# Kernel tuning notes

Hardware: AMD Instinct MI355X
Metric: run time of the kernel (lower is better)

Reference implementation:

```python
import jax, jax.numpy as jnp
import numpy as np

LMAX = 2
C1 = 64; C2 = 64; COUT = 64
B = 4096
SUM_RDIM = sum(3**L for L in range(LMAX + 1))   # 13
FEAT1 = C1 * SUM_RDIM                            # 832
FEAT2 = C2 * SUM_RDIM


def _enumerate_paths(Lmax):
    paths = []
    for L1 in range(Lmax + 1):
        for L2 in range(Lmax + 1):
            for k in range(min(L1, L2) + 1):
                Lout = L1 + L2 - 2 * k
                if 0 <= Lout <= Lmax:
                    paths.append((L1, L2, Lout, k, False))
            if L1 >= 1 and L2 >= 1:
                for k in range(min(L1 - 1, L2 - 1) + 1):
                    Lout = L1 + L2 - 2 * k - 1
                    if 0 <= Lout <= Lmax:
                        paths.append((L1, L2, Lout, k, True))
    return paths

PATHS = _enumerate_paths(LMAX)   # 15 paths for Lmax=2


def _path_eq(L1, L2, k, use_eps):
    # Fused equation: W[c,a,b] contracted together with the delta/eps path einsum.
    letters = list('defghijklmnopqrstuvwxyz')  # a,b,c reserved for channels
    i_idx = letters[:L1]
    j_idx = letters[L1:L1 + L2]
    for r in range(k):  # delta: contract last k indices of A with last k of B
        j_idx[L2 - k + r] = i_idx[L1 - k + r]
    i_free = i_idx[:L1 - k]
    j_free = j_idx[:L2 - k]
    eps_sub = None
    if use_eps:  # consume last free index of each side via eps_{p i j}
        p = letters[L1 + L2]
        eps_sub = p + i_free[-1] + j_free[-1]
        i_free, j_free = i_free[:-1], j_free[:-1]
        out = i_free + j_free + [p]
    else:
        out = i_free + j_free
    terms = ['cab', '...a' + ''.join(i_idx), '...b' + ''.join(j_idx)]
    if eps_sub is not None:
        terms.append(eps_sub)
    return ','.join(terms) + '->...c' + ''.join(out)


def _epsilon():
    e = np.zeros((3, 3, 3), dtype=np.float32)
    e[0, 1, 2] = e[1, 2, 0] = e[2, 0, 1] = 1.0
    e[2, 1, 0] = e[1, 0, 2] = e[0, 2, 1] = -1.0
    return jnp.asarray(e)


def _split_by_rank(x, C, Lmax):
    batch = x.shape[:-1]
    out, idx = {}, 0
    for L in range(Lmax + 1):
        d = C * 3**L
        blk = x[..., idx:idx + d]
        idx += d
        out[L] = blk.reshape(*batch, C) if L == 0 else blk.reshape(*batch, C, *((3,) * L))
    return out


def setup_inputs() -> dict:
    key = jax.random.key(0)
    k1, k2, k3 = jax.random.split(key, 3)
    x1 = jax.random.normal(k1, (B, FEAT1), dtype=jnp.float32)
    x2 = jax.random.normal(k2, (B, FEAT2), dtype=jnp.float32)
    weight = jax.random.normal(k3, (len(PATHS) * COUT * C1 * C2,), dtype=jnp.float32) * 0.02
    return {"x1": x1, "x2": x2, "weight": weight}


def reference(x1, x2, weight):
    A = _split_by_rank(x1, C1, LMAX)
    Bt = _split_by_rank(x2, C2, LMAX)
    eps = _epsilon().astype(x1.dtype)
    batch = x1.shape[:-1]
    blocks = {L: jnp.zeros((*batch, COUT) + (3,) * L, dtype=x1.dtype) for L in range(LMAX + 1)}
    wsz = COUT * C1 * C2
    for n, (L1, L2, Lout, k, use_eps) in enumerate(PATHS):
        Wp = weight[n * wsz:(n + 1) * wsz].reshape(COUT, C1, C2)
        eq = _path_eq(L1, L2, k, use_eps)
        ops = (Wp, A[L1], Bt[L2]) + ((eps,) if use_eps else ())
        blocks[Lout] = blocks[Lout] + jnp.einsum(eq, *ops, optimize='optimal')
    parts = [blocks[L].reshape(*batch, COUT * 3**L) for L in range(LMAX + 1)]
    return jnp.concatenate(parts, axis=-1)
```

## Files before the change

### kernel.cpp

```cpp
#include <hip/hip_runtime.h>
#include <cstdint>
#include <cstddef>


#define FEAT 832
#define ZT 64

typedef _Float16 half8 __attribute__((ext_vector_type(8)));
typedef float floatx16 __attribute__((ext_vector_type(16)));

struct Chunk {
  int wbase;
  int o1[3];
  int o2[3];
  float sg[3];
  int d1, d2, nt;
};

__global__ void swz_w_kernel(const float* __restrict__ w, _Float16* __restrict__ o) {
  const int i = blockIdx.x * 256 + threadIdx.x;
  const int lane = i & 63;
  const int pkc  = i >> 6;
  const int cgrp = pkc & 1;
  const int ksg  = (pkc >> 1) & 255;
  const int p    = pkc >> 9;
  const int c  = cgrp * 32 + (lane & 31);
  const int k0 = ksg * 16 + (lane >> 5) * 8;
  const float* src = w + (size_t)p * 262144 + (size_t)c * 4096 + k0;
  const float4 v0 = *(const float4*)(src);
  const float4 v1 = *(const float4*)(src + 4);
  half8 h = { (_Float16)v0.x, (_Float16)v0.y, (_Float16)v0.z, (_Float16)v0.w,
              (_Float16)v1.x, (_Float16)v1.y, (_Float16)v1.z, (_Float16)v1.w };
  *(half8*)(o + (size_t)i * 8) = h;
}

__global__ __launch_bounds__(256) void gather_kernel(
    float* __restrict__ out, const float* __restrict__ part, int np)
{
  __shared__ float T[64][65];
  const int zb = blockIdx.x * 64;
  const int fb = blockIdx.y * 64;
  const int tid = threadIdx.x;
  const int fl = tid >> 6;
  const int zl = tid & 63;
  #pragma unroll
  for (int i = 0; i < 16; ++i) {
    const int f = fb + fl + i * 4;
    int s, c;
    if (f < 64)       { s = 0;              c = f; }
    else if (f < 256) { const int g = f - 64;  c = g / 3; s = 1 + g % 3; }
    else              { const int g = f - 256; c = g / 9; s = 4 + g % 9; }
    const size_t base = (size_t)s * 262144 + (size_t)c * 4096 + zb + zl;
    float v = 0.0f;
    for (int q = 0; q < np; ++q)
      v += part[(size_t)q * 3407872 + base];
    T[fl + i * 4][zl] = v;
  }
  __syncthreads();
  const int zr = tid >> 6;
  const int fc = tid & 63;
  #pragma unroll
  for (int i = 0; i < 16; ++i) {
    const int z = zr + i * 4;
    float* o = out + (size_t)(zb + z) * FEAT + fb + fc;
    *o += T[fc][z];
  }
}

__device__ __forceinline__ half8 splat8(_Float16 h) {
  return half8{h, h, h, h, h, h, h, h};
}

template<int NT>
__device__ __forceinline__ void run_chunk(
    const Chunk C, const int zbase, const int ln31, const int hf,
    const int lane, const int tid, const int a0,
    const float* __restrict__ x1, const float* __restrict__ x2,
    const _Float16* __restrict__ Wh,
    _Float16* __restrict__ XS2, _Float16* __restrict__ XS1,
    floatx16& acc00, floatx16& acc01, floatx16& acc10, floatx16& acc11)
{
  __syncthreads();

  #pragma unroll
  for (int t = 0; t < NT; ++t) {
    const size_t base2 = (size_t)zbase * FEAT + C.o2[t];
    for (int e = tid; e < 4096; e += 128) {
      const int zz = e >> 6, b = e & 63;
      XS2[(t * 64 + zz) * 72 + b] =
          (_Float16)x2[base2 + (size_t)zz * FEAT + b * C.d2];
    }
  }
  #pragma unroll
  for (int t = 0; t < NT; ++t) {
    const float sgf = C.sg[t];
    const int o1 = C.o1[t];
    for (int e = tid; e < 4096; e += 128) {
      const int a = e & 63, zz = e >> 6;
      XS1[(t * 64 + a) * 66 + zz] =
          (_Float16)(x1[(size_t)(zbase + zz) * FEAT + o1 + a * C.d1] * sgf);
    }
  }
  __syncthreads();

  half8 x2r[NT][2][4];
  #pragma unroll
  for (int t = 0; t < NT; ++t)
    #pragma unroll
    for (int zh = 0; zh < 2; ++zh)
      #pragma unroll
      for (int ks = 0; ks < 4; ++ks)
        x2r[t][zh][ks] =
            *(const half8*)&XS2[(t * 64 + zh * 32 + ln31) * 72 + ks * 16 + hf * 8];

  const _Float16* __restrict__ Wq = Wh + C.wbase + lane * 8;
  const _Float16* __restrict__ Xq = XS1 + ln31;

  half8 afE[2][4], afO[2][4];
  const _Float16* __restrict__ w0 = Wq + (size_t)a0 * 4096;
  #pragma unroll
  for (int ks = 0; ks < 4; ++ks) {
    afE[0][ks] = *(const half8*)(w0 + ks * 1024);
    afE[1][ks] = *(const half8*)(w0 + ks * 1024 + 512);
    afO[0][ks] = *(const half8*)(w0 + 4096 + ks * 1024);
    afO[1][ks] = *(const half8*)(w0 + 4096 + ks * 1024 + 512);
  }
  _Float16 sc[NT][2], scn[NT][2];
  #pragma unroll
  for (int t = 0; t < NT; ++t)
    #pragma unroll
    for (int zh = 0; zh < 2; ++zh) {
      sc[t][zh]  = Xq[(t * 64 + a0) * 66 + zh * 32];
      scn[t][zh] = Xq[(t * 64 + a0 + 1) * 66 + zh * 32];
    }

  const int aend = a0 + 32;
  #pragma unroll 1
  for (int a = a0; a < aend; a += 2) {
    {
      half8 sv[NT][2];
      #pragma unroll
      for (int t = 0; t < NT; ++t) {
        sv[t][0] = splat8(sc[t][0]);
        sv[t][1] = splat8(sc[t][1]);
      }
      if (a + 2 < aend) {
        #pragma unroll
        for (int t = 0; t < NT; ++t) {
          sc[t][0] = Xq[(t * 64 + a + 2) * 66];
          sc[t][1] = Xq[(t * 64 + a + 2) * 66 + 32];
        }
      }
      #pragma unroll
      for (int ks = 0; ks < 4; ++ks) {
        half8 tb0 = sv[0][0] * x2r[0][0][ks];
        half8 tb1 = sv[0][1] * x2r[0][1][ks];
        if (NT > 1) { tb0 += sv[1][0] * x2r[1][0][ks]; tb1 += sv[1][1] * x2r[1][1][ks]; }
        if (NT > 2) { tb0 += sv[2][0] * x2r[2][0][ks]; tb1 += sv[2][1] * x2r[2][1][ks]; }
        acc00 = __builtin_amdgcn_mfma_f32_32x32x16_f16(afE[0][ks], tb0, acc00, 0, 0, 0);
        acc01 = __builtin_amdgcn_mfma_f32_32x32x16_f16(afE[0][ks], tb1, acc01, 0, 0, 0);
        acc10 = __builtin_amdgcn_mfma_f32_32x32x16_f16(afE[1][ks], tb0, acc10, 0, 0, 0);
        acc11 = __builtin_amdgcn_mfma_f32_32x32x16_f16(afE[1][ks], tb1, acc11, 0, 0, 0);
      }
      if (a + 2 < aend) {
        const _Float16* wn = Wq + (size_t)(a + 2) * 4096;
        #pragma unroll
        for (int ks = 0; ks < 4; ++ks) {
          afE[0][ks] = *(const half8*)(wn + ks * 1024);
          afE[1][ks] = *(const half8*)(wn + ks * 1024 + 512);
        }
      }
    }
    {
      half8 sv[NT][2];
      #pragma unroll
      for (int t = 0; t < NT; ++t) {
        sv[t][0] = splat8(scn[t][0]);
        sv[t][1] = splat8(scn[t][1]);
      }
      if (a + 3 < aend) {
        #pragma unroll
        for (int t = 0; t < NT; ++t) {
          scn[t][0] = Xq[(t * 64 + a + 3) * 66];
          scn[t][1] = Xq[(t * 64 + a + 3) * 66 + 32];
        }
      }
      #pragma unroll
      for (int ks = 0; ks < 4; ++ks) {
        half8 tb0 = sv[0][0] * x2r[0][0][ks];
        half8 tb1 = sv[0][1] * x2r[0][1][ks];
        if (NT > 1) { tb0 += sv[1][0] * x2r[1][0][ks]; tb1 += sv[1][1] * x2r[1][1][ks]; }
        if (NT > 2) { tb0 += sv[2][0] * x2r[2][0][ks]; tb1 += sv[2][1] * x2r[2][1][ks]; }
        acc00 = __builtin_amdgcn_mfma_f32_32x32x16_f16(afO[0][ks], tb0, acc00, 0, 0, 0);
        acc01 = __builtin_amdgcn_mfma_f32_32x32x16_f16(afO[0][ks], tb1, acc01, 0, 0, 0);
        acc10 = __builtin_amdgcn_mfma_f32_32x32x16_f16(afO[1][ks], tb0, acc10, 0, 0, 0);
        acc11 = __builtin_amdgcn_mfma_f32_32x32x16_f16(afO[1][ks], tb1, acc11, 0, 0, 0);
      }
      if (a + 3 < aend) {
        const _Float16* wn = Wq + (size_t)(a + 3) * 4096;
        #pragma unroll
        for (int ks = 0; ks < 4; ++ks) {
          afO[0][ks] = *(const half8*)(wn + ks * 1024);
          afO[1][ks] = *(const half8*)(wn + ks * 1024 + 512);
        }
      }
    }
  }
}

__global__ __launch_bounds__(128, 2) void tp_kernel(
    const float* __restrict__ x1, const float* __restrict__ x2,
    const _Float16* __restrict__ Wh, float* __restrict__ out,
    float* __restrict__ part)
{
  __shared__ __align__(16) _Float16 XS2[3 * 64 * 72];
  __shared__ __align__(16) _Float16 XS1[3 * 64 * 66];
  __shared__ Chunk chs[7];
  __shared__ int nch_s;

  const int tid  = threadIdx.x;
  const int slot = blockIdx.y;
  const int q    = blockIdx.z;
  const int nsplit = gridDim.z;
  const int zbase = blockIdx.x * ZT;
  const int ah   = tid >> 6;
  const int a0   = ah * 32;
  const int lane = tid & 63;
  const int ln31 = lane & 31;
  const int hf   = lane >> 5;

  int offO, dO, mO;
  if (slot == 0)      { offO = 0;   dO = 1; mO = 0; }
  else if (slot < 4)  { offO = 64;  dO = 3; mO = slot - 1; }
  else                { offO = 256; dO = 9; mO = slot - 4; }

  if (tid == 0) {
    int n = 0;
    auto add = [&](int p, int L1, int L2,
                   int i0, int i1, int i2, int j0, int j1, int j2,
                   float s0, float s1, float s2, int nt) {
      const int offs[3] = {0, 64, 256};
      const int ds[3]   = {1, 3, 9};
      Chunk c;
      c.wbase = p * 262144;
      c.o1[0] = offs[L1] + i0; c.o1[1] = offs[L1] + i1; c.o1[2] = offs[L1] + i2;
      c.o2[0] = offs[L2] + j0; c.o2[1] = offs[L2] + j1; c.o2[2] = offs[L2] + j2;
      c.sg[0] = s0; c.sg[1] = s1; c.sg[2] = s2;
      c.d1 = ds[L1]; c.d2 = ds[L2]; c.nt = nt;
      chs[n++] = c;
    };
    if (slot == 0) {
      add(0, 0,0, 0,0,0, 0,0,0, 1,0,0, 1);
      add(5, 1,1, 0,1,2, 0,1,2, 1,1,1, 3);
      add(13,2,2, 0,1,2, 0,1,2, 1,1,1, 3);
      add(13,2,2, 3,4,5, 3,4,5, 1,1,1, 3);
      add(13,2,2, 6,7,8, 6,7,8, 1,1,1, 3);
    } else if (slot < 4) {
      const int m = slot - 1, p1 = (m+1)%3, p2 = (m+2)%3;
      add(1, 0,1, 0,0,0, m,0,0, 1,0,0, 1);
      add(3, 1,0, m,0,0, 0,0,0, 1,0,0, 1);
      add(6, 1,1, p1,p2,0, p2,p1,0, 1,-1,0, 2);
      add(7, 1,2, 0,1,2, 3*m,3*m+1,3*m+2, 1,1,1, 3);
      add(10,2,1, 3*m,3*m+1,3*m+2, 0,1,2, 1,1,1, 3);
      add(14,2,2, 3*p1,3*p1+1,3*p1+2, 3*p2,3*p2+1,3*p2+2, 1,1,1, 3);
      add(14,2,2, 3*p2,3*p2+1,3*p2+2, 3*p1,3*p1+1,3*p1+2, -1,-1,-1, 3);
    } else {
      const int m = slot - 4, u = m/3, v = m%3, q1 = (v+1)%3, q2 = (v+2)%3;
      add(2, 0,2, 0,0,0, m,0,0, 1,0,0, 1);
      add(4, 1,1, u,0,0, v,0,0, 1,0,0, 1);
      add(8, 1,2, q1,q2,0, 3*u+q2,3*u+q1,0, 1,-1,0, 2);
      add(9, 2,0, m,0,0, 0,0,0, 1,0,0, 1);
      add(11,2,1, 3*u+q1,3*u+q2,0, q2,q1,0, 1,-1,0, 2);
      add(12,2,2, 3*u,3*u+1,3*u+2, 3*v,3*v+1,3*v+2, 1,1,1, 3);
    }
    nch_s = n;
  }
  __syncthreads();
  const int nch = nch_s;

  floatx16 acc00, acc01, acc10, acc11;
  #pragma unroll
  for (int r = 0; r < 16; ++r) {
    acc00[r] = 0.0f; acc01[r] = 0.0f; acc10[r] = 0.0f; acc11[r] = 0.0f;
  }

  for (int ci = q; ci < nch; ci += nsplit) {
    const Chunk C = chs[ci];
    if (C.nt == 1)
      run_chunk<1>(C, zbase, ln31, hf, lane, tid, a0, x1, x2, Wh, XS2, XS1,
                   acc00, acc01, acc10, acc11);
    else if (C.nt == 2)
      run_chunk<2>(C, zbase, ln31, hf, lane, tid, a0, x1, x2, Wh, XS2, XS1,
                   acc00, acc01, acc10, acc11);
    else
      run_chunk<3>(C, zbase, ln31, hf, lane, tid, a0, x1, x2, Wh, XS2, XS1,
                   acc00, acc01, acc10, acc11);
  }

  __syncthreads();
  float* R = (float*)XS2;
  if (ah == 1) {
    #pragma unroll
    for (int r = 0; r < 16; ++r) {
      R[(0 * 16 + r) * 64 + lane] = acc00[r];
      R[(1 * 16 + r) * 64 + lane] = acc01[r];
      R[(2 * 16 + r) * 64 + lane] = acc10[r];
      R[(3 * 16 + r) * 64 + lane] = acc11[r];
    }
  }
  __syncthreads();
  if (ah == 0) {
    #pragma unroll
    for (int r = 0; r < 16; ++r) {
      acc00[r] += R[(0 * 16 + r) * 64 + lane];
      acc01[r] += R[(1 * 16 + r) * 64 + lane];
      acc10[r] += R[(2 * 16 + r) * 64 + lane];
      acc11[r] += R[(3 * 16 + r) * 64 + lane];
    }

    if (q == 0) {
      float* __restrict__ op0 = out + (size_t)(zbase + ln31) * FEAT + offO + mO;
      float* __restrict__ op1 = out + (size_t)(zbase + 32 + ln31) * FEAT + offO + mO;
      #pragma unroll
      for (int r = 0; r < 16; ++r) {
        const int cr = (r & 3) + 8 * (r >> 2) + 4 * hf;
        op0[(size_t)cr * dO]        = acc00[r];
        op0[(size_t)(cr + 32) * dO] = acc10[r];
        op1[(size_t)cr * dO]        = acc01[r];
        op1[(size_t)(cr + 32) * dO] = acc11[r];
      }
    } else {
      float* __restrict__ op0 = part + (size_t)(q - 1) * 3407872
                                     + (size_t)slot * 262144 + (zbase + ln31);
      float* __restrict__ op1 = op0 + 32;
      #pragma unroll
      for (int r = 0; r < 16; ++r) {
        const int cr = (r & 3) + 8 * (r >> 2) + 4 * hf;
        op0[(size_t)cr * 4096]        = acc00[r];
        op0[(size_t)(cr + 32) * 4096] = acc10[r];
        op1[(size_t)cr * 4096]        = acc01[r];
        op1[(size_t)(cr + 32) * 4096] = acc11[r];
      }
    }
  }
}

extern "C" void kernel_launch(void* const* d_in, const int* in_sizes, int n_in,
                              void* d_out, int out_size, void* d_ws, size_t ws_size,
                              hipStream_t stream) {
  const float* x1 = (const float*)d_in[0];
  const float* x2 = (const float*)d_in[1];
  const float* w  = (const float*)d_in[2];
  float* out = (float*)d_out;
  _Float16* Wh = (_Float16*)d_ws;
  float* part = (float*)((char*)d_ws + 7864320);

  const size_t plane_bytes = 3407872ull * 4ull;
  int np = (ws_size > 7864320) ? (int)((ws_size - 7864320) / plane_bytes) : 1;
  if (np > 3) np = 3;
  if (np < 1) np = 1;
  const int nsplit = np + 1;

  const int nchunks = 15 * 64 * 4096 / 8;
  hipLaunchKernelGGL(swz_w_kernel, dim3(nchunks / 256), dim3(256), 0, stream, w, Wh);

  dim3 grid(64, 13, nsplit);
  hipLaunchKernelGGL(tp_kernel, grid, dim3(128), 0, stream, x1, x2, Wh, out, part);

  dim3 ggrid(64, 13);
  hipLaunchKernelGGL(gather_kernel, ggrid, dim3(256), 0, stream, out, part, np);
}
```

Baseline: 411.3 us.

## Split warps over output channels instead of the K dimension

Each of the two wavefronts now owns half of the 64 output channels and runs the full 64-step reduction over input channel a. Before, each wavefront covered all outputs over half of a, and the two partial sums were reduced through shared memory. This removes that LDS reduction, its two barriers and half the accumulator registers. In exchange, each wave does twice as many loop iterations and the B-operand product tb is computed twice, once per wave, for the same MFMA count.

```diff
diff --git a/kernel.cpp b/kernel.cpp
--- a/kernel.cpp
+++ b/kernel.cpp
@@ -74,11 +74,11 @@
 template<int NT>
 __device__ __forceinline__ void run_chunk(
     const Chunk C, const int zbase, const int ln31, const int hf,
-    const int lane, const int tid, const int a0,
+    const int lane, const int tid, const int cg,
     const float* __restrict__ x1, const float* __restrict__ x2,
     const _Float16* __restrict__ Wh,
     _Float16* __restrict__ XS2, _Float16* __restrict__ XS1,
-    floatx16& acc00, floatx16& acc01, floatx16& acc10, floatx16& acc11)
+    floatx16& acc0, floatx16& acc1)
 {
   __syncthreads();
 
@@ -113,30 +113,26 @@
         x2r[t][zh][ks] =
             *(const half8*)&XS2[(t * 64 + zh * 32 + ln31) * 72 + ks * 16 + hf * 8];
 
-  const _Float16* __restrict__ Wq = Wh + C.wbase + lane * 8;
+  const _Float16* __restrict__ Wq = Wh + C.wbase + cg * 512 + lane * 8;
   const _Float16* __restrict__ Xq = XS1 + ln31;
 
-  half8 afE[2][4], afO[2][4];
-  const _Float16* __restrict__ w0 = Wq + (size_t)a0 * 4096;
+  half8 afE[4], afO[4];
   #pragma unroll
   for (int ks = 0; ks < 4; ++ks) {
-    afE[0][ks] = *(const half8*)(w0 + ks * 1024);
-    afE[1][ks] = *(const half8*)(w0 + ks * 1024 + 512);
-    afO[0][ks] = *(const half8*)(w0 + 4096 + ks * 1024);
-    afO[1][ks] = *(const half8*)(w0 + 4096 + ks * 1024 + 512);
+    afE[ks] = *(const half8*)(Wq + ks * 1024);
+    afO[ks] = *(const half8*)(Wq + 4096 + ks * 1024);
   }
   _Float16 sc[NT][2], scn[NT][2];
   #pragma unroll
   for (int t = 0; t < NT; ++t)
     #pragma unroll
     for (int zh = 0; zh < 2; ++zh) {
-      sc[t][zh]  = Xq[(t * 64 + a0) * 66 + zh * 32];
-      scn[t][zh] = Xq[(t * 64 + a0 + 1) * 66 + zh * 32];
-    }
-
-  const int aend = a0 + 32;
+      sc[t][zh]  = Xq[(t * 64 + 0) * 66 + zh * 32];
+      scn[t][zh] = Xq[(t * 64 + 1) * 66 + zh * 32];
+    }
+
   #pragma unroll 1
-  for (int a = a0; a < aend; a += 2) {
+  for (int a = 0; a < 64; a += 2) {
     {
       half8 sv[NT][2];
       #pragma unroll
@@ -144,7 +140,7 @@
         sv[t][0] = splat8(sc[t][0]);
         sv[t][1] = splat8(sc[t][1]);
       }
-      if (a + 2 < aend) {
+      if (a + 2 < 64) {
         #pragma unroll
         for (int t = 0; t < NT; ++t) {
           sc[t][0] = Xq[(t * 64 + a + 2) * 66];
@@ -157,18 +153,14 @@
         half8 tb1 = sv[0][1] * x2r[0][1][ks];
         if (NT > 1) { tb0 += sv[1][0] * x2r[1][0][ks]; tb1 += sv[1][1] * x2r[1][1][ks]; }
         if (NT > 2) { tb0 += sv[2][0] * x2r[2][0][ks]; tb1 += sv[2][1] * x2r[2][1][ks]; }
-        acc00 = __builtin_amdgcn_mfma_f32_32x32x16_f16(afE[0][ks], tb0, acc00, 0, 0, 0);
-        acc01 = __builtin_amdgcn_mfma_f32_32x32x16_f16(afE[0][ks], tb1, acc01, 0, 0, 0);
-        acc10 = __builtin_amdgcn_mfma_f32_32x32x16_f16(afE[1][ks], tb0, acc10, 0, 0, 0);
-        acc11 = __builtin_amdgcn_mfma_f32_32x32x16_f16(afE[1][ks], tb1, acc11, 0, 0, 0);
-      }
-      if (a + 2 < aend) {
+        acc0 = __builtin_amdgcn_mfma_f32_32x32x16_f16(afE[ks], tb0, acc0, 0, 0, 0);
+        acc1 = __builtin_amdgcn_mfma_f32_32x32x16_f16(afE[ks], tb1, acc1, 0, 0, 0);
+      }
+      if (a + 2 < 64) {
         const _Float16* wn = Wq + (size_t)(a + 2) * 4096;
         #pragma unroll
-        for (int ks = 0; ks < 4; ++ks) {
-          afE[0][ks] = *(const half8*)(wn + ks * 1024);
-          afE[1][ks] = *(const half8*)(wn + ks * 1024 + 512);
-        }
+        for (int ks = 0; ks < 4; ++ks)
+          afE[ks] = *(const half8*)(wn + ks * 1024);
       }
     }
     {
@@ -178,7 +170,7 @@
         sv[t][0] = splat8(scn[t][0]);
         sv[t][1] = splat8(scn[t][1]);
       }
-      if (a + 3 < aend) {
+      if (a + 3 < 64) {
         #pragma unroll
         for (int t = 0; t < NT; ++t) {
           scn[t][0] = Xq[(t * 64 + a + 3) * 66];
@@ -191,18 +183,14 @@
         half8 tb1 = sv[0][1] * x2r[0][1][ks];
         if (NT > 1) { tb0 += sv[1][0] * x2r[1][0][ks]; tb1 += sv[1][1] * x2r[1][1][ks]; }
         if (NT > 2) { tb0 += sv[2][0] * x2r[2][0][ks]; tb1 += sv[2][1] * x2r[2][1][ks]; }
-        acc00 = __builtin_amdgcn_mfma_f32_32x32x16_f16(afO[0][ks], tb0, acc00, 0, 0, 0);
-        acc01 = __builtin_amdgcn_mfma_f32_32x32x16_f16(afO[0][ks], tb1, acc01, 0, 0, 0);
-        acc10 = __builtin_amdgcn_mfma_f32_32x32x16_f16(afO[1][ks], tb0, acc10, 0, 0, 0);
-        acc11 = __builtin_amdgcn_mfma_f32_32x32x16_f16(afO[1][ks], tb1, acc11, 0, 0, 0);
-      }
-      if (a + 3 < aend) {
+        acc0 = __builtin_amdgcn_mfma_f32_32x32x16_f16(afO[ks], tb0, acc0, 0, 0, 0);
+        acc1 = __builtin_amdgcn_mfma_f32_32x32x16_f16(afO[ks], tb1, acc1, 0, 0, 0);
+      }
+      if (a + 3 < 64) {
         const _Float16* wn = Wq + (size_t)(a + 3) * 4096;
         #pragma unroll
-        for (int ks = 0; ks < 4; ++ks) {
-          afO[0][ks] = *(const half8*)(wn + ks * 1024);
-          afO[1][ks] = *(const half8*)(wn + ks * 1024 + 512);
-        }
+        for (int ks = 0; ks < 4; ++ks)
+          afO[ks] = *(const half8*)(wn + ks * 1024);
       }
     }
   }
@@ -223,8 +211,7 @@
   const int q    = blockIdx.z;
   const int nsplit = gridDim.z;
   const int zbase = blockIdx.x * ZT;
-  const int ah   = tid >> 6;
-  const int a0   = ah * 32;
+  const int cg   = tid >> 6;
   const int lane = tid & 63;
   const int ln31 = lane & 31;
   const int hf   = lane >> 5;
@@ -278,69 +265,38 @@
   __syncthreads();
   const int nch = nch_s;
 
-  floatx16 acc00, acc01, acc10, acc11;
-  #pragma unroll
-  for (int r = 0; r < 16; ++r) {
-    acc00[r] = 0.0f; acc01[r] = 0.0f; acc10[r] = 0.0f; acc11[r] = 0.0f;
-  }
+  floatx16 acc0, acc1;
+  #pragma unroll
+  for (int r = 0; r < 16; ++r) { acc0[r] = 0.0f; acc1[r] = 0.0f; }
 
   for (int ci = q; ci < nch; ci += nsplit) {
     const Chunk C = chs[ci];
     if (C.nt == 1)
-      run_chunk<1>(C, zbase, ln31, hf, lane, tid, a0, x1, x2, Wh, XS2, XS1,
-                   acc00, acc01, acc10, acc11);
+      run_chunk<1>(C, zbase, ln31, hf, lane, tid, cg, x1, x2, Wh, XS2, XS1, acc0, acc1);
     else if (C.nt == 2)
-      run_chunk<2>(C, zbase, ln31, hf, lane, tid, a0, x1, x2, Wh, XS2, XS1,
-                   acc00, acc01, acc10, acc11);
+      run_chunk<2>(C, zbase, ln31, hf, lane, tid, cg, x1, x2, Wh, XS2, XS1, acc0, acc1);
     else
-      run_chunk<3>(C, zbase, ln31, hf, lane, tid, a0, x1, x2, Wh, XS2, XS1,
-                   acc00, acc01, acc10, acc11);
-  }
-
-  __syncthreads();
-  float* R = (float*)XS2;
-  if (ah == 1) {
+      run_chunk<3>(C, zbase, ln31, hf, lane, tid, cg, x1, x2, Wh, XS2, XS1, acc0, acc1);
+  }
+
+  if (q == 0) {
+    float* __restrict__ op0 = out + (size_t)(zbase + ln31) * FEAT + offO + mO;
+    float* __restrict__ op1 = out + (size_t)(zbase + 32 + ln31) * FEAT + offO + mO;
     #pragma unroll
     for (int r = 0; r < 16; ++r) {
-      R[(0 * 16 + r) * 64 + lane] = acc00[r];
-      R[(1 * 16 + r) * 64 + lane] = acc01[r];
-      R[(2 * 16 + r) * 64 + lane] = acc10[r];
-      R[(3 * 16 + r) * 64 + lane] = acc11[r];
-    }
-  }
-  __syncthreads();
-  if (ah == 0) {
+      const int cr = cg * 32 + (r & 3) + 8 * (r >> 2) + 4 * hf;
+      op0[(size_t)cr * dO] = acc0[r];
+      op1[(size_t)cr * dO] = acc1[r];
+    }
+  } else {
+    float* __restrict__ op0 = part + (size_t)(q - 1) * 3407872
+                                   + (size_t)slot * 262144 + (zbase + ln31);
+    float* __restrict__ op1 = op0 + 32;
     #pragma unroll
     for (int r = 0; r < 16; ++r) {
-      acc00[r] += R[(0 * 16 + r) * 64 + lane];
-      acc01[r] += R[(1 * 16 + r) * 64 + lane];
-      acc10[r] += R[(2 * 16 + r) * 64 + lane];
-      acc11[r] += R[(3 * 16 + r) * 64 + lane];
-    }
-
-    if (q == 0) {
-      float* __restrict__ op0 = out + (size_t)(zbase + ln31) * FEAT + offO + mO;
-      float* __restrict__ op1 = out + (size_t)(zbase + 32 + ln31) * FEAT + offO + mO;
-      #pragma unroll
-      for (int r = 0; r < 16; ++r) {
-        const int cr = (r & 3) + 8 * (r >> 2) + 4 * hf;
-        op0[(size_t)cr * dO]        = acc00[r];
-        op0[(size_t)(cr + 32) * dO] = acc10[r];
-        op1[(size_t)cr * dO]        = acc01[r];
-        op1[(size_t)(cr + 32) * dO] = acc11[r];
-      }
-    } else {
-      float* __restrict__ op0 = part + (size_t)(q - 1) * 3407872
-                                     + (size_t)slot * 262144 + (zbase + ln31);
-      float* __restrict__ op1 = op0 + 32;
-      #pragma unroll
-      for (int r = 0; r < 16; ++r) {
-        const int cr = (r & 3) + 8 * (r >> 2) + 4 * hf;
-        op0[(size_t)cr * 4096]        = acc00[r];
-        op0[(size_t)(cr + 32) * 4096] = acc10[r];
-        op1[(size_t)cr * 4096]        = acc01[r];
-        op1[(size_t)(cr + 32) * 4096] = acc11[r];
-      }
+      const int cr = cg * 32 + (r & 3) + 8 * (r >> 2) + 4 * hf;
+      op0[(size_t)cr * 4096] = acc0[r];
+      op1[(size_t)cr * 4096] = acc1[r];
     }
   }
 }
```

Measured after the change: 374.4 us. 9.0% less time.
